# Kernel tuning notes

Measured on AMD Instinct MI355X. Metric: run time of the kernel, lower is better.

The kernel has to match this reference:

```python
import jax, jax.numpy as jnp
import numpy as np

B = 8
SEQ = 8192
D_MODEL = 256
D_STATE = 64
D_CONV = 4
EXPAND = 4
HEADDIM = 64
N_LAYERS = 8
D_INNER = EXPAND * D_MODEL            # 1024
NHEADS = D_INNER // HEADDIM           # 16
CONV_DIM = D_INNER + 2 * D_STATE      # 1152 (ngroups=1)
D_IN_PROJ = 2 * D_INNER + 2 * D_STATE + NHEADS  # 2192


def setup_inputs():
    key = jax.random.key(0)
    ks = jax.random.split(key, 16)
    rn = lambda k, shape, fan: jax.random.normal(k, shape, jnp.float32) / np.float32(np.sqrt(fan))
    inp = {}
    inp["x"] = jax.random.normal(ks[0], (B, 3, SEQ), jnp.float32)
    inp["conv1_w"] = rn(ks[1], (64, 3, 16), 3 * 16)
    inp["conv1_b"] = rn(ks[2], (64,), 64)
    inp["conv2_w"] = rn(ks[3], (D_MODEL, 64, 16), 64 * 16)
    inp["conv2_b"] = rn(ks[4], (D_MODEL,), D_MODEL)
    inp["in_proj_w"] = rn(ks[5], (N_LAYERS, D_IN_PROJ, D_MODEL), D_MODEL)
    inp["dw_conv_w"] = rn(ks[6], (N_LAYERS, CONV_DIM, D_CONV), D_CONV)
    inp["dw_conv_b"] = rn(ks[7], (N_LAYERS, CONV_DIM), D_CONV)
    inp["dt_bias"] = jax.random.normal(ks[8], (N_LAYERS, NHEADS), jnp.float32) * 0.5
    inp["A_log"] = jax.random.uniform(ks[9], (N_LAYERS, NHEADS), jnp.float32, 0.0, 2.0)
    inp["ssm_D"] = jnp.ones((N_LAYERS, NHEADS), jnp.float32)
    inp["rms_w"] = jnp.ones((N_LAYERS, D_INNER), jnp.float32)
    inp["out_proj_w"] = rn(ks[10], (N_LAYERS, D_MODEL, D_INNER), D_INNER)
    inp["ln_w"] = jnp.ones((D_MODEL,), jnp.float32)
    inp["ln_b"] = jnp.zeros((D_MODEL,), jnp.float32)
    inp["reg1_w"] = rn(ks[11], (128, D_MODEL), D_MODEL)
    inp["reg1_b"] = rn(ks[12], (128,), 128)
    inp["reg2_w"] = rn(ks[13], (1, 128), 128)
    inp["reg2_b"] = rn(ks[14], (1,), 128)
    return inp


def _silu(v):
    return v * jax.nn.sigmoid(v)


def _mamba2_layer(u, in_proj_w, dw_w, dw_b, dt_bias, A_log, ssm_D, rms_w, out_proj_w):
    b, l, _ = u.shape
    zxbcdt = u @ in_proj_w.T                               # (b,l,2192)
    z = zxbcdt[..., :D_INNER]
    xBC = zxbcdt[..., D_INNER:D_INNER + CONV_DIM]
    dt = jax.nn.softplus(zxbcdt[..., D_INNER + CONV_DIM:] + dt_bias)   # (b,l,h)
    # causal depthwise conv1d (kernel D_CONV), then SiLU
    pad = jnp.pad(xBC, ((0, 0), (D_CONV - 1, 0), (0, 0)))
    conv = sum(pad[:, k:k + l, :] * dw_w[:, k] for k in range(D_CONV)) + dw_b
    xBC = _silu(conv)
    xh = xBC[..., :D_INNER].reshape(b, l, NHEADS, HEADDIM)  # (b,l,h,p)
    Bm = xBC[..., D_INNER:D_INNER + D_STATE]                # (b,l,n)
    Cm = xBC[..., D_INNER + D_STATE:]                       # (b,l,n)
    dA = jnp.exp(dt * (-jnp.exp(A_log)))                    # (b,l,h)

    def step(h, inp):
        dA_t, dt_t, x_t, B_t, C_t = inp
        h = h * dA_t[:, :, None, None] + (dt_t[:, :, None] * x_t)[..., None] * B_t[:, None, None, :]
        y = jnp.einsum('bhpn,bn->bhp', h, C_t)
        return h, y

    h0 = jnp.zeros((b, NHEADS, HEADDIM, D_STATE), u.dtype)
    xs = (dA.transpose(1, 0, 2), dt.transpose(1, 0, 2),
          xh.transpose(1, 0, 2, 3), Bm.transpose(1, 0, 2), Cm.transpose(1, 0, 2))
    _, ys = jax.lax.scan(step, h0, xs)                      # (l,b,h,p)
    y = ys.transpose(1, 0, 2, 3) + ssm_D[None, None, :, None] * xh
    y = y.reshape(b, l, D_INNER)
    y = y * _silu(z)                                        # gated
    y = y * jax.lax.rsqrt(jnp.mean(y * y, axis=-1, keepdims=True) + 1e-5) * rms_w
    return y @ out_proj_w.T


def reference(x, conv1_w, conv1_b, conv2_w, conv2_b, in_proj_w, dw_conv_w, dw_conv_b,
              dt_bias, A_log, ssm_D, rms_w, out_proj_w, ln_w, ln_b,
              reg1_w, reg1_b, reg2_w, reg2_b):
    dn = ('NCH', 'OIH', 'NCH')
    h = jax.lax.conv_general_dilated(x, conv1_w, (4,), [(6, 6)], dimension_numbers=dn) + conv1_b[None, :, None]
    h = jax.nn.gelu(h, approximate=False)
    h = jax.lax.conv_general_dilated(h, conv2_w, (2,), [(7, 7)], dimension_numbers=dn) + conv2_b[None, :, None]
    h = jax.nn.gelu(h, approximate=False)
    h = h.transpose(0, 2, 1)                                # (b, 1024, d_model)
    for i in range(N_LAYERS):
        h = _mamba2_layer(h, in_proj_w[i], dw_conv_w[i], dw_conv_b[i],
                          dt_bias[i], A_log[i], ssm_D[i], rms_w[i], out_proj_w[i])
    mu = jnp.mean(h, -1, keepdims=True)
    var = jnp.mean((h - mu) ** 2, -1, keepdims=True)
    h = (h - mu) * jax.lax.rsqrt(var + 1e-5) * ln_w + ln_b  # LayerNorm
    pooled = h.mean(1)
    r = jax.nn.gelu(pooled @ reg1_w.T + reg1_b, approximate=False)
    return r @ reg2_w.T + reg2_b                            # (b, 1)
```

## Files before the change

### kernel.cpp

```cpp
#include <hip/hip_runtime.h>
#include <math.h>

#define NB       8
#define SEQ      8192
#define L1OUT    2048
#define LOUT     1024
#define DMODEL   256
#define DINNER   1024
#define NHEADS   16
#define HEADDIM  64
#define DSTATE   64
#define CONVDIM  1152
#define DINPROJ  2192
#define NPADIN   2304
#define NLAYERS  8
#define NCHUNK   16
#define Q        64

#define N_CAST1 (NLAYERS * NPADIN * DMODEL)
#define N_CAST2 (NLAYERS * DMODEL * DINNER)
#define N_CAST3 (DMODEL * 1024)

typedef _Float16 f16;
typedef __attribute__((ext_vector_type(8))) _Float16 f16x8;
typedef __attribute__((ext_vector_type(4))) _Float16 f16x4;
typedef __attribute__((ext_vector_type(4))) float    f32x4;

__device__ __forceinline__ float gelu_f(float v) {
    return 0.5f * v * (1.0f + erff(v * 0.70710678118654752f));
}
__device__ __forceinline__ float silu_f(float v) {
    return v * __builtin_amdgcn_rcpf(1.0f + __expf(-v));
}

__device__ __forceinline__ void gload16(const void* g, void* l) {
    __builtin_amdgcn_global_load_lds(
        (const __attribute__((address_space(1))) unsigned int*)g,
        (__attribute__((address_space(3))) unsigned int*)l, 16, 0, 0);
}

__device__ __forceinline__ int xcd_chunk(int flat, int nblk) {
    return (flat & 7) * (nblk >> 3) + (flat >> 3);
}

__global__ __launch_bounds__(256) void k_castall(const float* __restrict__ w_in,
                                                 const float* __restrict__ w_out,
                                                 const float* __restrict__ rmsw,
                                                 const float* __restrict__ w_c2,
                                                 f16* __restrict__ o_in,
                                                 f16* __restrict__ o_out,
                                                 f16* __restrict__ o_c2) {
    int idx = blockIdx.x * 256 + threadIdx.x;
    if (idx < N_CAST1) {
        int c = idx & 255;
        int r = (idx >> 8) % NPADIN;
        int l = idx / (NPADIN * 256);
        float v = (r < DINPROJ) ? w_in[((size_t)l * DINPROJ + r) * 256 + c] : 0.f;
        o_in[idx] = (f16)v;
    } else if (idx < N_CAST1 + N_CAST2) {
        int i = idx - N_CAST1;
        int k = i % DINNER;
        int l = i / (DMODEL * DINNER);
        o_out[i] = (f16)(w_out[i] * rmsw[l * DINNER + k]);
    } else if (idx < N_CAST1 + N_CAST2 + N_CAST3) {
        int i = idx - N_CAST1 - N_CAST2;
        o_c2[i] = (f16)w_c2[i];
    }
}

__global__ __launch_bounds__(256) void k_conv1(const float* __restrict__ x,
                                               const float* __restrict__ w,
                                               const float* __restrict__ bias,
                                               f16* __restrict__ out) {
    int idx = blockIdx.x * 256 + threadIdx.x;
    int u  = idx & 255;
    int co = (idx >> 8) & 63;
    int b  = idx >> 14;
    int xbase = u * 32 - 8;

    float acc[8];
#pragma unroll
    for (int t = 0; t < 8; ++t) acc[t] = bias[co];

#pragma unroll
    for (int ci = 0; ci < 3; ++ci) {
        const float* xp = x + ((size_t)b * 3 + ci) * SEQ;
        float xb[48];
#pragma unroll
        for (int j = 0; j < 12; ++j) {
            int off = xbase + j * 4;
            float4 v;
            if (off >= 0 && off + 3 < SEQ) {
                v = *(const float4*)&xp[off];
            } else {
                v.x = (off + 0 >= 0 && off + 0 < SEQ) ? xp[off + 0] : 0.f;
                v.y = (off + 1 >= 0 && off + 1 < SEQ) ? xp[off + 1] : 0.f;
                v.z = (off + 2 >= 0 && off + 2 < SEQ) ? xp[off + 2] : 0.f;
                v.w = (off + 3 >= 0 && off + 3 < SEQ) ? xp[off + 3] : 0.f;
            }
            xb[j * 4 + 0] = v.x; xb[j * 4 + 1] = v.y;
            xb[j * 4 + 2] = v.z; xb[j * 4 + 3] = v.w;
        }
        const float* wp = w + (co * 3 + ci) * 16;
        float wv[16];
#pragma unroll
        for (int k = 0; k < 16; ++k) wv[k] = wp[k];
#pragma unroll
        for (int t = 0; t < 8; ++t)
#pragma unroll
            for (int k = 0; k < 16; ++k)
                acc[t] = fmaf(xb[t * 4 + k + 2], wv[k], acc[t]);
    }
    f16x8 o;
#pragma unroll
    for (int t = 0; t < 8; ++t) o[t] = (f16)gelu_f(acc[t]);
    *(f16x8*)&out[((size_t)(b * 64 + co)) * L1OUT + u * 8] = o;
}

__global__ __launch_bounds__(256) void k_im2col(const f16* __restrict__ h1,
                                                f16* __restrict__ A) {
    int idx = blockIdx.x * 256 + threadIdx.x;
    int g = idx & 127;
    int row = idx >> 7;
    int t = row & (LOUT - 1);
    int b = row >> 10;
    int ci = g >> 1, k0 = (g & 1) * 8;
    int pos0 = t * 2 + k0 - 7;
    const f16* hp = h1 + ((size_t)(b * 64 + ci)) * L1OUT;
    f16x8 v;
#pragma unroll
    for (int j = 0; j < 8; ++j) {
        int p = pos0 + j;
        v[j] = (p >= 0 && p < L1OUT) ? hp[p] : (f16)0.f;
    }
    *(f16x8*)&A[(size_t)row * 1024 + g * 8] = v;
}

template<int BM, int EPI>
__global__ __launch_bounds__(256) void k_hgemm(const f16* __restrict__ A,
                                               const f16* __restrict__ Bw,
                                               f16* __restrict__ Ch,
                                               int M, int N, int K,
                                               const float* __restrict__ bias,
                                               const float* __restrict__ dt_bias,
                                               const float* __restrict__ A_log,
                                               float* __restrict__ dadt) {
    constexpr int MI = BM / 32;
    __shared__ f16 As[BM * 64];
    __shared__ f16 Bs[128 * 64];
    int tid  = threadIdx.x;
    int lane = tid & 63, wid = tid >> 6;
    int wm = wid >> 1, wn = wid & 1;

    int nbx = gridDim.x;
    int flat = blockIdx.y * nbx + blockIdx.x;
    int logical = xcd_chunk(flat, nbx * gridDim.y);
    int row0 = (logical / nbx) * BM, col0 = (logical % nbx) * 128;
    int lr = lane & 15, kb = lane >> 4;

    f32x4 acc[MI][4];
#pragma unroll
    for (int mi = 0; mi < MI; ++mi)
#pragma unroll
        for (int ni = 0; ni < 4; ++ni)
            acc[mi][ni] = (f32x4){0.f, 0.f, 0.f, 0.f};

    int sr  = tid >> 3;
    int scx = ((tid & 7) ^ (sr & 7)) * 8;
    int rsw = (lr & 7) * 8;

    for (int k0 = 0; k0 < K; k0 += 64) {
        __syncthreads();
#pragma unroll
        for (int is = 0; is < BM / 32; ++is)
            gload16(A + (size_t)(row0 + is * 32 + sr) * K + k0 + scx,
                    &As[is * 2048 + wid * 512]);
#pragma unroll
        for (int is = 0; is < 4; ++is)
            gload16(Bw + (size_t)(col0 + is * 32 + sr) * K + k0 + scx,
                    &Bs[is * 2048 + wid * 512]);
        __syncthreads();

#pragma unroll
        for (int ks = 0; ks < 2; ++ks) {
            int cbase = (ks * 32 + kb * 8) ^ rsw;
            f16x8 a[MI], b[4];
#pragma unroll
            for (int mi = 0; mi < MI; ++mi)
                a[mi] = *reinterpret_cast<const f16x8*>(
                    &As[(wm * (BM / 2) + mi * 16 + lr) * 64 + cbase]);
#pragma unroll
            for (int ni = 0; ni < 4; ++ni)
                b[ni] = *reinterpret_cast<const f16x8*>(
                    &Bs[(wn * 64 + ni * 16 + lr) * 64 + cbase]);
#pragma unroll
            for (int mi = 0; mi < MI; ++mi)
#pragma unroll
                for (int ni = 0; ni < 4; ++ni)
                    acc[mi][ni] = __builtin_amdgcn_mfma_f32_16x16x32_f16(
                        a[mi], b[ni], acc[mi][ni], 0, 0, 0);
        }
    }

#pragma unroll
    for (int mi = 0; mi < MI; ++mi)
#pragma unroll
        for (int ni = 0; ni < 4; ++ni) {
            int ccol = col0 + wn * 64 + ni * 16 + lr;
            if (ccol < N) {
                int rbase = row0 + wm * (BM / 2) + mi * 16 + kb * 4;
                f32x4 v = acc[mi][ni];
#pragma unroll
                for (int r = 0; r < 4; ++r) {
                    float val = v[r];
                    if (EPI == 1) val = gelu_f(val + bias[ccol]);
                    Ch[(size_t)(rbase + r) * N + ccol] = (f16)val;
                    if (EPI == 2 && ccol >= DINNER + CONVDIM) {
                        int hh = ccol - (DINNER + CONVDIM);
                        float raw = val + dt_bias[hh];
                        float dtv = (raw > 20.f) ? raw : log1pf(__expf(raw));
                        float lda = -__expf(A_log[hh]) * dtv;
                        *(float2*)&dadt[(size_t)(rbase + r) * 32 + hh * 2] =
                            make_float2(lda, dtv);
                    }
                }
            }
        }
}

__global__ __launch_bounds__(256) void k_ssd1(const f16* __restrict__ zx16,
                                              const float* __restrict__ dadt,
                                              const float* __restrict__ dw_w,
                                              const float* __restrict__ dw_b,
                                              const float* __restrict__ ssmD,
                                              f16* __restrict__ y1,
                                              f16* __restrict__ Sbuf16,
                                              float* __restrict__ Abuf,
                                              f16* __restrict__ C16) {
    __shared__ f16 Bs[64][72];
    __shared__ f16 Cs[64][72];
    __shared__ float GT[64][68];
    __shared__ f16 Mw[4][64][72];
    __shared__ float2 LaDt[4][64];

    int tid = threadIdx.x, lane = tid & 63, wid = tid >> 6;
    int bid = xcd_chunk(blockIdx.x, NB * NCHUNK * 4);
    int hq = bid & 3, c = (bid >> 2) & 15, b = bid >> 6;
    int h = hq * 4 + wid;
    int lr = lane & 15, kb = lane >> 4;
    f16* Xs = &Mw[0][0][0];

    {
        int sg = tid % 48;
        int ts = tid / 48;
        if (ts < 4) {
            int xc;
            if (sg < 32)      xc = hq * 256 + sg * 8;
            else if (sg < 40) xc = 1024 + (sg - 32) * 8;
            else              xc = 1088 + (sg - 40) * 8;
            int zc = 1024 + xc;
            float4 wv[8];
            float  bv[8];
#pragma unroll
            for (int j = 0; j < 8; ++j) {
                wv[j] = *(const float4*)&dw_w[(xc + j) * 4];
                bv[j] = dw_b[xc + j];
            }
            int l0 = c * 64 + ts * 16;
            const f16* zrow = zx16 + ((size_t)(b * 1024 + l0)) * DINPROJ + zc;
            f16x8 r0, r1, r2, r3;
            f16x8 zz;
#pragma unroll
            for (int j = 0; j < 8; ++j) zz[j] = (f16)0.f;
            r0 = (l0 >= 3) ? *(const f16x8*)(zrow - 3 * DINPROJ) : zz;
            r1 = (l0 >= 2) ? *(const f16x8*)(zrow - 2 * DINPROJ) : zz;
            r2 = (l0 >= 1) ? *(const f16x8*)(zrow - 1 * DINPROJ) : zz;
#pragma unroll
            for (int t = 0; t < 16; ++t) {
                r3 = *(const f16x8*)(zrow + t * DINPROJ);
                f16x8 o;
#pragma unroll
                for (int j = 0; j < 8; ++j) {
                    float s = bv[j];
                    s = fmaf((float)r0[j], wv[j].x, s);
                    s = fmaf((float)r1[j], wv[j].y, s);
                    s = fmaf((float)r2[j], wv[j].z, s);
                    s = fmaf((float)r3[j], wv[j].w, s);
                    o[j] = (f16)silu_f(s);
                }
                int row = ts * 16 + t;
                if (sg < 32) {
                    f16x4 o0 = {o[0], o[1], o[2], o[3]};
                    f16x4 o1 = {o[4], o[5], o[6], o[7]};
                    *(f16x4*)&Xs[row * 260 + sg * 8]     = o0;
                    *(f16x4*)&Xs[row * 260 + sg * 8 + 4] = o1;
                } else if (sg < 40) {
                    *(f16x8*)&Bs[row][(sg - 32) * 8] = o;
                } else {
                    *(f16x8*)&Cs[row][(sg - 40) * 8] = o;
                }
                r0 = r1; r1 = r2; r2 = r3;
            }
        }
    }

    float2 ad = *(const float2*)&dadt[((size_t)(b * 1024 + c * 64 + lane) * 16 + h) * 2];
    float La = ad.x;
#pragma unroll
    for (int o = 1; o < 64; o <<= 1) {
        float v = __shfl_up(La, o);
        if (lane >= o) La += v;
    }
    float dt_own = ad.y;
    float La63 = __shfl(La, 63);
    float w_own = __expf(La63 - La) * dt_own;
    LaDt[wid][lane] = make_float2(La, dt_own);
    float Dh = ssmD[h];
    __syncthreads();

    if (hq == 0) {
        f16* cp = C16 + (((size_t)(b * 16 + c)) << 12);
#pragma unroll
        for (int it = 0; it < 2; ++it) {
            int cid = it * 256 + tid;
            int row = cid >> 3, off = (cid & 7) * 8;
            *(f16x8*)&cp[row * 64 + off] = *(const f16x8*)&Cs[row][off];
        }
    }

    f16x8 xfrag[4][2];
#pragma unroll
    for (int pi = 0; pi < 4; ++pi)
#pragma unroll
        for (int ks = 0; ks < 2; ++ks) {
            f16x8 v;
#pragma unroll
            for (int j = 0; j < 8; ++j)
                v[j] = Xs[(ks * 32 + kb * 8 + j) * 260 + wid * 64 + pi * 16 + lr];
            xfrag[pi][ks] = v;
        }

    {
        int tq = wid & 1, sq = wid >> 1;
        f32x4 g[2][2];
#pragma unroll
        for (int i = 0; i < 2; ++i)
#pragma unroll
            for (int j = 0; j < 2; ++j) g[i][j] = (f32x4){0.f, 0.f, 0.f, 0.f};
#pragma unroll
        for (int ks = 0; ks < 2; ++ks) {
            f16x8 a[2], bb[2];
#pragma unroll
            for (int ti = 0; ti < 2; ++ti)
                a[ti] = *(const f16x8*)&Cs[tq * 32 + ti * 16 + lr][ks * 32 + kb * 8];
#pragma unroll
            for (int si = 0; si < 2; ++si)
                bb[si] = *(const f16x8*)&Bs[sq * 32 + si * 16 + lr][ks * 32 + kb * 8];
#pragma unroll
            for (int ti = 0; ti < 2; ++ti)
#pragma unroll
                for (int si = 0; si < 2; ++si)
                    g[ti][si] = __builtin_amdgcn_mfma_f32_16x16x32_f16(
                        a[ti], bb[si], g[ti][si], 0, 0, 0);
        }
#pragma unroll
        for (int ti = 0; ti < 2; ++ti)
#pragma unroll
            for (int si = 0; si < 2; ++si)
#pragma unroll
                for (int r = 0; r < 4; ++r)
                    GT[sq * 32 + si * 16 + lr][tq * 32 + ti * 16 + kb * 4 + r] = g[ti][si][r];
    }
    __syncthreads();

    {
        f16x8 brow[8];
#pragma unroll
        for (int i = 0; i < 8; ++i) brow[i] = *(const f16x8*)&Bs[lane][i * 8];
#pragma unroll
        for (int i = 0; i < 8; ++i)
#pragma unroll
            for (int j = 0; j < 8; ++j)
                Mw[wid][i * 8 + j][lane] = (f16)((float)brow[i][j] * w_own);
    }
    __builtin_amdgcn_wave_barrier();

    f16x8 sbfrag[4][2];
#pragma unroll
    for (int ni = 0; ni < 4; ++ni)
#pragma unroll
        for (int ks = 0; ks < 2; ++ks)
            sbfrag[ni][ks] = *(const f16x8*)&Mw[wid][ni * 16 + lr][ks * 32 + kb * 8];

    {
        f32x4 accS[4][4];
#pragma unroll
        for (int pi = 0; pi < 4; ++pi)
#pragma unroll
            for (int ni = 0; ni < 4; ++ni) accS[pi][ni] = (f32x4){0.f, 0.f, 0.f, 0.f};
#pragma unroll
        for (int ks = 0; ks < 2; ++ks)
#pragma unroll
            for (int pi = 0; pi < 4; ++pi)
#pragma unroll
                for (int ni = 0; ni < 4; ++ni)
                    accS[pi][ni] = __builtin_amdgcn_mfma_f32_16x16x32_f16(
                        xfrag[pi][ks], sbfrag[ni][ks], accS[pi][ni], 0, 0, 0);
        size_t sbase = ((size_t)((b * 16 + h) * 16 + c)) << 12;
#pragma unroll
        for (int pi = 0; pi < 4; ++pi)
#pragma unroll
            for (int ni = 0; ni < 4; ++ni)
#pragma unroll
                for (int r = 0; r < 4; ++r)
                    Sbuf16[sbase + (size_t)(pi * 16 + kb * 4 + r) * 64 + ni * 16 + lr] =
                        (f16)accS[pi][ni][r];
        if (lane == 0) Abuf[(b * 16 + h) * 16 + c] = __expf(La63);
    }
    __builtin_amdgcn_wave_barrier();

    {
        int t = lane;
        float la_t = La;
#pragma unroll
        for (int s8 = 0; s8 < 8; ++s8) {
            f16x8 mv;
#pragma unroll
            for (int j = 0; j < 8; ++j) {
                int s = s8 * 8 + j;
                float2 ld = LaDt[wid][s];
                float m = (s <= t) ? GT[s][t] * __expf(la_t - ld.x) * ld.y : 0.f;
                if (s == t) m += Dh;
                mv[j] = (f16)m;
            }
            *(f16x8*)&Mw[wid][t][s8 * 8] = mv;
        }
    }
    __builtin_amdgcn_wave_barrier();

    {
        f32x4 accY[4][4];
#pragma unroll
        for (int ti = 0; ti < 4; ++ti)
#pragma unroll
            for (int pi = 0; pi < 4; ++pi) accY[ti][pi] = (f32x4){0.f, 0.f, 0.f, 0.f};
#pragma unroll
        for (int ks = 0; ks < 2; ++ks) {
            f16x8 af[4];
#pragma unroll
            for (int ti = 0; ti < 4; ++ti)
                af[ti] = *(const f16x8*)&Mw[wid][ti * 16 + lr][ks * 32 + kb * 8];
#pragma unroll
            for (int ti = 0; ti < 4; ++ti)
#pragma unroll
                for (int pi = 0; pi < 4; ++pi)
                    accY[ti][pi] = __builtin_amdgcn_mfma_f32_16x16x32_f16(
                        af[ti], xfrag[pi][ks], accY[ti][pi], 0, 0, 0);
        }
        f16* yp = y1 + ((size_t)(b * 1024 + c * 64)) * 1024 + h * 64;
#pragma unroll
        for (int ti = 0; ti < 4; ++ti)
#pragma unroll
            for (int pi = 0; pi < 4; ++pi)
#pragma unroll
                for (int r = 0; r < 4; ++r)
                    yp[(size_t)(ti * 16 + kb * 4 + r) * 1024 + pi * 16 + lr] =
                        (f16)accY[ti][pi][r];
    }
}

__global__ __launch_bounds__(256) void k_ssd2f(const f16* __restrict__ C16,
                                               const f16* __restrict__ Sbuf16,
                                               const float* __restrict__ Abuf,
                                               const float* __restrict__ dadt,
                                               f16* __restrict__ y2) {
    __shared__ f16 Hs[NCHUNK][1024];
    int tid = threadIdx.x, lane = tid & 63, wv = tid >> 6;
    int bid = xcd_chunk(blockIdx.x, NB * NHEADS * 4);
    int ph = bid & 3, h = (bid >> 2) & 15, b = bid >> 6;
    int bh = b * 16 + h;
    int lr = lane & 15, kb = lane >> 4;
    size_t base = ((size_t)bh << 16) + ph * 1024;

    {
        int lp = tid >> 4;
        int n0 = (tid & 15) * 4;
        int dst = lp * 64 + ((((n0 >> 3) ^ (lp & 7))) << 3) + (n0 & 7);
        float Hl[4];
#pragma unroll
        for (int j = 0; j < 4; ++j) Hl[j] = 0.f;
#pragma unroll
        for (int c = 0; c < NCHUNK; ++c) {
            f16x4 o;
#pragma unroll
            for (int j = 0; j < 4; ++j) o[j] = (f16)Hl[j];
            *(f16x4*)&Hs[c][dst] = o;
            float A = Abuf[bh * 16 + c];
            f16x4 s = *(const f16x4*)&Sbuf16[base + (size_t)c * 4096 + lp * 64 + n0];
#pragma unroll
            for (int j = 0; j < 4; ++j)
                Hl[j] = fmaf(Hl[j], A, (float)s[j]);
        }
    }
    __syncthreads();

    const f16* cpb = C16 + ((size_t)b << 16);
#pragma unroll
    for (int i = 0; i < 4; ++i) {
        int c = wv * 4 + i;
        float2 ad = *(const float2*)&dadt[((size_t)(b * 1024 + c * 64 + lane) * 16 + h) * 2];
        float La = ad.x;
#pragma unroll
        for (int o = 1; o < 64; o <<= 1) {
            float v = __shfl_up(La, o);
            if (lane >= o) La += v;
        }

        f16x8 hfrag[2];
#pragma unroll
        for (int ks = 0; ks < 2; ++ks) {
            int cf = (ks * 32 + kb * 8) ^ ((lr & 7) * 8);
            hfrag[ks] = *(const f16x8*)&Hs[c][lr * 64 + cf];
        }

        const f16* cp = cpb + ((size_t)c << 12);
        f32x4 acc[4];
#pragma unroll
        for (int ti = 0; ti < 4; ++ti) acc[ti] = (f32x4){0.f, 0.f, 0.f, 0.f};
#pragma unroll
        for (int ks = 0; ks < 2; ++ks) {
            f16x8 af[4];
#pragma unroll
            for (int ti = 0; ti < 4; ++ti)
                af[ti] = *(const f16x8*)(cp + (ti * 16 + lr) * 64 + ks * 32 + kb * 8);
#pragma unroll
            for (int ti = 0; ti < 4; ++ti)
                acc[ti] = __builtin_amdgcn_mfma_f32_16x16x32_f16(
                    af[ti], hfrag[ks], acc[ti], 0, 0, 0);
        }
        f16* yp = y2 + ((size_t)(b * 1024 + c * 64)) * 1024 + h * 64 + ph * 16;
#pragma unroll
        for (int ti = 0; ti < 4; ++ti)
#pragma unroll
            for (int r = 0; r < 4; ++r) {
                int t = ti * 16 + kb * 4 + r;
                float sc = __expf(__shfl(La, t));
                yp[(size_t)t * 1024 + lr] = (f16)(sc * acc[ti][r]);
            }
    }
}

__global__ __launch_bounds__(256) void k_goproj(const f16* __restrict__ y1,
                                                const f16* __restrict__ y2,
                                                const f16* __restrict__ zx16,
                                                const f16* __restrict__ Bw,
                                                f16* __restrict__ out) {
    __shared__ f16 Bs[256 * 64];
    __shared__ f16 Ag[32 * 64];
    int tid = threadIdx.x, lane = tid & 63, wv = tid >> 6;
    int row0 = xcd_chunk(blockIdx.x, 256) * 32;
    int lr = lane & 15, kb = lane >> 4;
    int row = tid >> 3, seg = tid & 7;

    f16x8 vreg[16];
    float ss = 0.f;
    {
        const f16* p1 = y1 + (size_t)(row0 + row) * DINNER;
        const f16* p2 = y2 + (size_t)(row0 + row) * DINNER;
        const f16* pz = zx16 + (size_t)(row0 + row) * DINPROJ;
#pragma unroll
        for (int kc = 0; kc < 16; ++kc) {
            int c = kc * 64 + seg * 8;
            f16x8 a = *(const f16x8*)(p1 + c);
            f16x8 b = *(const f16x8*)(p2 + c);
            f16x8 z = *(const f16x8*)(pz + c);
            f16x8 o;
#pragma unroll
            for (int j = 0; j < 8; ++j) {
                float v = ((float)a[j] + (float)b[j]) * silu_f((float)z[j]);
                ss += v * v;
                o[j] = (f16)v;
            }
            vreg[kc] = o;
        }
        ss += __shfl_xor(ss, 1);
        ss += __shfl_xor(ss, 2);
        ss += __shfl_xor(ss, 4);
    }
    float rnorm = rsqrtf(ss * (1.f / DINNER) + 1e-5f);

    int sr  = tid >> 3;
    int scx = ((tid & 7) ^ (sr & 7)) * 8;
    int rsw = (lr & 7) * 8;
    int agw = (seg ^ (row & 7)) * 8;

    f32x4 acc[2][4];
#pragma unroll
    for (int mi = 0; mi < 2; ++mi)
#pragma unroll
        for (int ni = 0; ni < 4; ++ni)
            acc[mi][ni] = (f32x4){0.f, 0.f, 0.f, 0.f};

#pragma unroll
    for (int kc = 0; kc < 16; ++kc) {
        int k0 = kc * 64;
        __syncthreads();
#pragma unroll
        for (int is = 0; is < 8; ++is)
            gload16(Bw + (size_t)(is * 32 + sr) * DINNER + k0 + scx,
                    &Bs[is * 2048 + wv * 512]);
        {
            f16x8 o;
#pragma unroll
            for (int j = 0; j < 8; ++j)
                o[j] = (f16)((float)vreg[kc][j] * rnorm);
            *(f16x8*)&Ag[row * 64 + agw] = o;
        }
        __syncthreads();

#pragma unroll
        for (int ks = 0; ks < 2; ++ks) {
            int cb = (ks * 32 + kb * 8) ^ rsw;
            f16x8 a0 = *(const f16x8*)&Ag[lr * 64 + cb];
            f16x8 a1 = *(const f16x8*)&Ag[(16 + lr) * 64 + cb];
            f16x8 bfr[4];
#pragma unroll
            for (int ni = 0; ni < 4; ++ni)
                bfr[ni] = *(const f16x8*)&Bs[(wv * 64 + ni * 16 + lr) * 64 + cb];
#pragma unroll
            for (int ni = 0; ni < 4; ++ni) {
                acc[0][ni] = __builtin_amdgcn_mfma_f32_16x16x32_f16(
                    a0, bfr[ni], acc[0][ni], 0, 0, 0);
                acc[1][ni] = __builtin_amdgcn_mfma_f32_16x16x32_f16(
                    a1, bfr[ni], acc[1][ni], 0, 0, 0);
            }
        }
    }

#pragma unroll
    for (int mi = 0; mi < 2; ++mi)
#pragma unroll
        for (int ni = 0; ni < 4; ++ni) {
            int ccol = wv * 64 + ni * 16 + lr;
#pragma unroll
            for (int r = 0; r < 4; ++r)
                out[(size_t)(row0 + mi * 16 + kb * 4 + r) * DMODEL + ccol] =
                    (f16)acc[mi][ni][r];
        }
}

__global__ __launch_bounds__(256) void k_lnpool(const f16* __restrict__ h,
                                                const float* __restrict__ lnw,
                                                const float* __restrict__ lnb,
                                                float* __restrict__ pooledp) {
    __shared__ float pl[4][256];
    int bid = blockIdx.x;
    int b = bid >> 5, seg = bid & 31;
    int tid = threadIdx.x, lane = tid & 63, w = tid >> 6;
    int c4 = lane * 4;
    float4 lw = *(const float4*)&lnw[c4];
    float4 lb = *(const float4*)&lnb[c4];
    float acc0 = 0.f, acc1 = 0.f, acc2 = 0.f, acc3 = 0.f;
    const f16* hb = h + ((size_t)b * 1024 + seg * 32 + w * 8) * DMODEL;
#pragma unroll
    for (int i = 0; i < 8; ++i) {
        f16x4 hv = *(const f16x4*)(hb + (size_t)i * DMODEL + c4);
        float vx = (float)hv.x, vy = (float)hv.y, vz = (float)hv.z, vw = (float)hv.w;
        float s1 = vx + vy + vz + vw;
        float s2 = vx * vx + vy * vy + vz * vz + vw * vw;
#pragma unroll
        for (int o = 32; o > 0; o >>= 1) {
            s1 += __shfl_xor(s1, o);
            s2 += __shfl_xor(s2, o);
        }
        float mu = s1 * (1.f / DMODEL);
        float var = s2 * (1.f / DMODEL) - mu * mu;
        float rr = rsqrtf(var + 1e-5f);
        acc0 += (vx - mu) * rr * lw.x + lb.x;
        acc1 += (vy - mu) * rr * lw.y + lb.y;
        acc2 += (vz - mu) * rr * lw.z + lb.z;
        acc3 += (vw - mu) * rr * lw.w + lb.w;
    }
    pl[w][c4 + 0] = acc0; pl[w][c4 + 1] = acc1;
    pl[w][c4 + 2] = acc2; pl[w][c4 + 3] = acc3;
    __syncthreads();
    float tot = pl[0][tid] + pl[1][tid] + pl[2][tid] + pl[3][tid];
    pooledp[(size_t)(b * 32 + seg) * 256 + tid] = tot;
}

__global__ __launch_bounds__(128) void k_head(const float* __restrict__ pooledp,
                                              const float* __restrict__ w1,
                                              const float* __restrict__ b1,
                                              const float* __restrict__ w2,
                                              const float* __restrict__ b2,
                                              float* __restrict__ out) {
    __shared__ float sp[256];
    __shared__ float red[2];
    int b = blockIdx.x, j = threadIdx.x;
    for (int d = j; d < 256; d += 128) {
        float s = 0.f;
#pragma unroll
        for (int seg = 0; seg < 32; ++seg)
            s += pooledp[(size_t)(b * 32 + seg) * 256 + d];
        sp[d] = s * (1.f / LOUT);
    }
    __syncthreads();
    float acc = b1[j];
#pragma unroll 8
    for (int d = 0; d < DMODEL; ++d)
        acc = fmaf(sp[d], w1[j * DMODEL + d], acc);
    float r = gelu_f(acc) * w2[j];
#pragma unroll
    for (int o = 32; o > 0; o >>= 1) r += __shfl_down(r, o, 64);
    int lane = j & 63, wid = j >> 6;
    if (lane == 0) red[wid] = r;
    __syncthreads();
    if (j == 0) out[b] = red[0] + red[1] + b2[0];
}

extern "C" void kernel_launch(void* const* d_in, const int* in_sizes, int n_in,
                              void* d_out, int out_size, void* d_ws, size_t ws_size,
                              hipStream_t stream) {
    const float* x         = (const float*)d_in[0];
    const float* conv1_w   = (const float*)d_in[1];
    const float* conv1_b   = (const float*)d_in[2];
    const float* conv2_w   = (const float*)d_in[3];
    const float* conv2_b   = (const float*)d_in[4];
    const float* in_proj_w = (const float*)d_in[5];
    const float* dw_w      = (const float*)d_in[6];
    const float* dw_b      = (const float*)d_in[7];
    const float* dt_bias   = (const float*)d_in[8];
    const float* A_log     = (const float*)d_in[9];
    const float* ssm_D     = (const float*)d_in[10];
    const float* rms_w     = (const float*)d_in[11];
    const float* out_proj_w= (const float*)d_in[12];
    const float* ln_w      = (const float*)d_in[13];
    const float* ln_b      = (const float*)d_in[14];
    const float* reg1_w    = (const float*)d_in[15];
    const float* reg1_b    = (const float*)d_in[16];
    const float* reg2_w    = (const float*)d_in[17];
    const float* reg2_b    = (const float*)d_in[18];

    float* ws = (float*)d_ws;
    size_t off = 0;
    float* dadt    = ws + off; off += (size_t)NB * LOUT * NHEADS * 2;
    float* Abuf    = ws + off; off += (size_t)NB * NHEADS * NCHUNK;
    float* pooledp = ws + off; off += (size_t)NB * 32 * 256;

    f16* fbase = (f16*)(ws + off);
    size_t foff = 0;
    f16* c1f16  = fbase + foff; foff += (size_t)NB * 64 * L1OUT;
    f16* hbf0   = fbase + foff; foff += (size_t)NB * LOUT * DMODEL;
    f16* hbf1   = fbase + foff; foff += (size_t)NB * LOUT * DMODEL;
    f16* y2     = fbase + foff; foff += (size_t)NB * LOUT * DINNER;
    f16* y1     = fbase + foff; foff += (size_t)NB * LOUT * DINNER;
    f16* C16    = fbase + foff; foff += (size_t)NB * NCHUNK * 64 * 64;
    f16* zx16   = fbase + foff; foff += (size_t)NB * LOUT * DINPROJ;
    f16* Sbuf16 = fbase + foff; foff += (size_t)NB * NHEADS * NCHUNK * 4096;
    f16* w_in_h = fbase + foff; foff += (size_t)NLAYERS * NPADIN * DMODEL;
    f16* w_out_h= fbase + foff; foff += (size_t)NLAYERS * DMODEL * DINNER;
    f16* w_c2_h = fbase + foff; foff += (size_t)DMODEL * 1024;
    f16* im2h   = y1;

    {
        int total = N_CAST1 + N_CAST2 + N_CAST3;
        k_castall<<<(total + 255) / 256, 256, 0, stream>>>(
            in_proj_w, out_proj_w, rms_w, conv2_w, w_in_h, w_out_h, w_c2_h);
    }

    k_conv1<<<(NB * 64 * 256) / 256, 256, 0, stream>>>(x, conv1_w, conv1_b, c1f16);
    k_im2col<<<(NB * LOUT * 128) / 256, 256, 0, stream>>>(c1f16, im2h);
    {
        dim3 g(256 / 128, 8192 / 64);
        k_hgemm<64, 1><<<g, 256, 0, stream>>>(im2h, w_c2_h, hbf0,
                                              8192, 256, 1024, conv2_b,
                                              nullptr, nullptr, nullptr);
    }

    f16* hcur = hbf0;
    f16* hnxt = hbf1;
    for (int i = 0; i < NLAYERS; ++i) {
        {
            dim3 g(NPADIN / 128, 8192 / 128);
            k_hgemm<128, 2><<<g, 256, 0, stream>>>(
                hcur, w_in_h + (size_t)i * NPADIN * DMODEL, zx16,
                8192, DINPROJ, DMODEL, nullptr,
                dt_bias + i * NHEADS, A_log + i * NHEADS, dadt);
        }
        k_ssd1<<<NB * NCHUNK * 4, 256, 0, stream>>>(
            zx16, dadt, dw_w + (size_t)i * CONVDIM * 4, dw_b + (size_t)i * CONVDIM,
            ssm_D + i * NHEADS, y1, Sbuf16, Abuf, C16);
        k_ssd2f<<<NB * NHEADS * 4, 256, 0, stream>>>(C16, Sbuf16, Abuf, dadt, y2);
        k_goproj<<<8192 / 32, 256, 0, stream>>>(
            y1, y2, zx16, w_out_h + (size_t)i * DMODEL * DINNER, hnxt);
        f16* tmp = hcur; hcur = hnxt; hnxt = tmp;
    }

    k_lnpool<<<NB * 32, 256, 0, stream>>>(hcur, ln_w, ln_b, pooledp);
    k_head<<<NB, 128, 0, stream>>>(pooledp, reg1_w, reg1_b, reg2_w, reg2_b, (float*)d_out);
}
```

Before: 839.5 us.

## Add dedicated in-projection GEMM with full-K LDS staging and fused SiLU on z

Replaces the generic templated GEMM for the per-layer in-projection with a specialized kernel that loads the whole K=256 slice of A (64 rows) and B (128 cols) into swizzled LDS at once and runs all MFMA steps without a K loop. It switches to 64-row tiles, doubling the number of blocks. It also applies SiLU to the z columns in the GEMM epilogue, so the gated output-projection kernel no longer computes silu(z). The costs are about 96KB of LDS per block, which may limit occupancy, and storing silu(z) in fp16 instead of raw z.

```diff
diff --git a/kernel.cpp b/kernel.cpp
--- a/kernel.cpp
+++ b/kernel.cpp
@@ -141,10 +141,7 @@
                                                const f16* __restrict__ Bw,
                                                f16* __restrict__ Ch,
                                                int M, int N, int K,
-                                               const float* __restrict__ bias,
-                                               const float* __restrict__ dt_bias,
-                                               const float* __restrict__ A_log,
-                                               float* __restrict__ dadt) {
+                                               const float* __restrict__ bias) {
     constexpr int MI = BM / 32;
     __shared__ f16 As[BM * 64];
     __shared__ f16 Bs[128 * 64];
@@ -215,7 +212,87 @@
                     float val = v[r];
                     if (EPI == 1) val = gelu_f(val + bias[ccol]);
                     Ch[(size_t)(rbase + r) * N + ccol] = (f16)val;
-                    if (EPI == 2 && ccol >= DINNER + CONVDIM) {
+                }
+            }
+        }
+}
+
+__global__ __launch_bounds__(256) void k_inproj(const f16* __restrict__ A,
+                                                const f16* __restrict__ Bw,
+                                                f16* __restrict__ Ch,
+                                                const float* __restrict__ dt_bias,
+                                                const float* __restrict__ A_log,
+                                                float* __restrict__ dadt) {
+    __shared__ f16 As[64 * 256];
+    __shared__ f16 Bs[128 * 256];
+    int tid  = threadIdx.x;
+    int lane = tid & 63, wid = tid >> 6;
+    int wm = wid >> 1, wn = wid & 1;
+
+    constexpr int NBX = NPADIN / 128;
+    int flat = blockIdx.y * NBX + blockIdx.x;
+    int logical = xcd_chunk(flat, NBX * (8192 / 64));
+    int row0 = (logical / NBX) * 64, col0 = (logical % NBX) * 128;
+    int lr = lane & 15, kb = lane >> 4;
+
+#pragma unroll
+    for (int i = 0; i < 8; ++i) {
+        int flt = i * 256 + tid;
+        int row = flt >> 5, ch = flt & 31;
+        gload16(A + (size_t)(row0 + row) * DMODEL + ((ch ^ (row & 7)) * 8),
+                &As[(size_t)flt * 8]);
+    }
+#pragma unroll
+    for (int i = 0; i < 16; ++i) {
+        int flt = i * 256 + tid;
+        int row = flt >> 5, ch = flt & 31;
+        gload16(Bw + (size_t)(col0 + row) * DMODEL + ((ch ^ (row & 7)) * 8),
+                &Bs[(size_t)flt * 8]);
+    }
+    __syncthreads();
+
+    f32x4 acc[2][4];
+#pragma unroll
+    for (int mi = 0; mi < 2; ++mi)
+#pragma unroll
+        for (int ni = 0; ni < 4; ++ni)
+            acc[mi][ni] = (f32x4){0.f, 0.f, 0.f, 0.f};
+
+    int rsw = (lr & 7) * 8;
+#pragma unroll
+    for (int ks = 0; ks < 8; ++ks) {
+        int cbase = (ks * 32 + kb * 8) ^ rsw;
+        f16x8 a[2], b[4];
+#pragma unroll
+        for (int mi = 0; mi < 2; ++mi)
+            a[mi] = *reinterpret_cast<const f16x8*>(
+                &As[(wm * 32 + mi * 16 + lr) * 256 + cbase]);
+#pragma unroll
+        for (int ni = 0; ni < 4; ++ni)
+            b[ni] = *reinterpret_cast<const f16x8*>(
+                &Bs[(wn * 64 + ni * 16 + lr) * 256 + cbase]);
+#pragma unroll
+        for (int mi = 0; mi < 2; ++mi)
+#pragma unroll
+            for (int ni = 0; ni < 4; ++ni)
+                acc[mi][ni] = __builtin_amdgcn_mfma_f32_16x16x32_f16(
+                    a[mi], b[ni], acc[mi][ni], 0, 0, 0);
+    }
+
+#pragma unroll
+    for (int mi = 0; mi < 2; ++mi)
+#pragma unroll
+        for (int ni = 0; ni < 4; ++ni) {
+            int ccol = col0 + wn * 64 + ni * 16 + lr;
+            if (ccol < DINPROJ) {
+                int rbase = row0 + wm * 32 + mi * 16 + kb * 4;
+                f32x4 v = acc[mi][ni];
+#pragma unroll
+                for (int r = 0; r < 4; ++r) {
+                    float val = v[r];
+                    float st = (ccol < DINNER) ? silu_f(val) : val;
+                    Ch[(size_t)(rbase + r) * DINPROJ + ccol] = (f16)st;
+                    if (ccol >= DINNER + CONVDIM) {
                         int hh = ccol - (DINNER + CONVDIM);
                         float raw = val + dt_bias[hh];
                         float dtv = (raw > 20.f) ? raw : log1pf(__expf(raw));
@@ -577,7 +654,7 @@
             f16x8 o;
 #pragma unroll
             for (int j = 0; j < 8; ++j) {
-                float v = ((float)a[j] + (float)b[j]) * silu_f((float)z[j]);
+                float v = ((float)a[j] + (float)b[j]) * (float)z[j];
                 ss += v * v;
                 o[j] = (f16)v;
             }
@@ -773,18 +850,16 @@
     {
         dim3 g(256 / 128, 8192 / 64);
         k_hgemm<64, 1><<<g, 256, 0, stream>>>(im2h, w_c2_h, hbf0,
-                                              8192, 256, 1024, conv2_b,
-                                              nullptr, nullptr, nullptr);
+                                              8192, 256, 1024, conv2_b);
     }
 
     f16* hcur = hbf0;
     f16* hnxt = hbf1;
     for (int i = 0; i < NLAYERS; ++i) {
         {
-            dim3 g(NPADIN / 128, 8192 / 128);
-            k_hgemm<128, 2><<<g, 256, 0, stream>>>(
+            dim3 g(NPADIN / 128, 8192 / 64);
+            k_inproj<<<g, 256, 0, stream>>>(
                 hcur, w_in_h + (size_t)i * NPADIN * DMODEL, zx16,
-                8192, DINPROJ, DMODEL, nullptr,
                 dt_bias + i * NHEADS, A_log + i * NHEADS, dadt);
         }
         k_ssd1<<<NB * NCHUNK * 4, 256, 0, stream>>>(
```

After: 924.4 us. 10.1% more time.
